# Kernel optimization log

Measured on AMD Instinct MI355X. Metric: run time of the kernel, lower is better.

Reference implementation:

```python
import jax, jax.numpy as jnp
import numpy as np

B, C = 8192, 128  # batch (edges/nodes), channels


def setup_inputs() -> dict:
    key = jax.random.key(0)
    k1, k2 = jax.random.split(key)
    T1 = jax.random.normal(k1, (B, C, 3, 3, 3), dtype=jnp.float32)
    T2 = jax.random.normal(k2, (B, C, 3, 3, 3), dtype=jnp.float32)
    return {"T1": T1, "T2": T2}


def reference(T1, T2):
    # BroadcastTC with r_1 = r_2 = 3 and three contractions (k = 1, 2, 3).
    # Original code permutes contracted axes of T1 to the back and of T2 to
    # the front, broadcasts an outer product, and sums the k contracted axes.
    # That is exactly a batched tensor contraction; we express it with einsum
    # (same math, no materialized broadcast product). Normalizer = 1/sqrt(3^k).
    # k=1: contract last axis of T1 with first feature axis of T2 -> rank-4 output
    out1 = jnp.einsum('bcxyk,bckuv->bcxyuv', T1, T2) * np.float32(1.0 / np.sqrt(3.0))
    # k=2: contract last two axes of T1 with first two feature axes of T2 -> rank-2
    out2 = jnp.einsum('bcxkl,bcklu->bcxu', T1, T2) * np.float32(1.0 / 3.0)
    # k=3: full contraction -> rank-0 (scalar per batch/channel)
    out3 = jnp.einsum('bcklm,bcklm->bc', T1, T2) * np.float32(1.0 / np.sqrt(27.0))
    return (out1, out2, out3)
```

## Files before the change

kernel.cpp:

```cpp
#include <hip/hip_runtime.h>


#define TPB 256
#define PPB 256

constexpr int  NPAIR    = 8192 * 128;
constexpr long OUT2_OFF = (long)NPAIR * 81;
constexpr long OUT3_OFF = OUT2_OFF + (long)NPAIR * 9;

__global__ __launch_bounds__(TPB)
void btc_kernel(const float* __restrict__ T1, const float* __restrict__ T2,
                float* __restrict__ out)
{
    __shared__ __align__(16) float lds[PPB * 27];

    const int  tid      = threadIdx.x;
    const long pairBase = (long)blockIdx.x * PPB;

    {
        const float4* g = reinterpret_cast<const float4*>(T1 + pairBase * 27);
        float4*       l = reinterpret_cast<float4*>(lds);
        #pragma unroll
        for (int i = 0; i < 7; ++i) {
            int idx = tid + i * TPB;
            if (idx < (PPB * 27) / 4) l[idx] = g[idx];
        }
    }
    __syncthreads();
    float a[27];
    #pragma unroll
    for (int j = 0; j < 27; ++j) a[j] = lds[tid * 27 + j];
    __syncthreads();

    {
        const float4* g = reinterpret_cast<const float4*>(T2 + pairBase * 27);
        float4*       l = reinterpret_cast<float4*>(lds);
        #pragma unroll
        for (int i = 0; i < 7; ++i) {
            int idx = tid + i * TPB;
            if (idx < (PPB * 27) / 4) l[idx] = g[idx];
        }
    }
    __syncthreads();
    float b[27];
    #pragma unroll
    for (int j = 0; j < 27; ++j) b[j] = lds[tid * 27 + j];
    __syncthreads();

    const float n1 = 0.57735026918962576f;
    const float n2 = 0.33333333333333333f;
    const float n3 = 0.19245008972987526f;

    #pragma unroll 1
    for (int g = 0; g < 4; ++g) {
        if ((tid >> 6) == g) {
            const int lp = tid & 63;
            #pragma unroll
            for (int x = 0; x < 3; ++x)
                #pragma unroll
                for (int y = 0; y < 3; ++y)
                    #pragma unroll
                    for (int u = 0; u < 3; ++u)
                        #pragma unroll
                        for (int v = 0; v < 3; ++v) {
                            float s = a[x*9 + y*3 + 0] * b[ 0 + u*3 + v]
                                    + a[x*9 + y*3 + 1] * b[ 9 + u*3 + v]
                                    + a[x*9 + y*3 + 2] * b[18 + u*3 + v];
                            lds[lp * 81 + x*27 + y*9 + u*3 + v] = s * n1;
                        }
        }
        __syncthreads();
        {
            const float4* ls = reinterpret_cast<const float4*>(lds);
            float4*       go = reinterpret_cast<float4*>(out + (pairBase + g * 64) * 81);
            #pragma unroll
            for (int k = 0; k < 6; ++k) {
                int idx = tid + k * TPB;
                if (idx < 1296) go[idx] = ls[idx];
            }
        }
        __syncthreads();
    }

    #pragma unroll
    for (int x = 0; x < 3; ++x) {
        #pragma unroll
        for (int u = 0; u < 3; ++u) {
            float s = 0.f;
            #pragma unroll
            for (int k = 0; k < 3; ++k)
                #pragma unroll
                for (int l = 0; l < 3; ++l)
                    s += a[x*9 + k*3 + l] * b[k*9 + l*3 + u];
            lds[tid * 9 + x*3 + u] = s * n2;
        }
    }
    __syncthreads();
    {
        const float4* ls = reinterpret_cast<const float4*>(lds);
        float4*       go = reinterpret_cast<float4*>(out + OUT2_OFF + pairBase * 9);
        #pragma unroll
        for (int k = 0; k < 3; ++k) {
            int idx = tid + k * TPB;
            if (idx < 576) go[idx] = ls[idx];
        }
    }

    float s3 = 0.f;
    #pragma unroll
    for (int j = 0; j < 27; ++j) s3 += a[j] * b[j];
    out[OUT3_OFF + pairBase + tid] = s3 * n3;
}

extern "C" void kernel_launch(void* const* d_in, const int* in_sizes, int n_in,
                              void* d_out, int out_size, void* d_ws, size_t ws_size,
                              hipStream_t stream)
{
    const float* T1  = (const float*)d_in[0];
    const float* T2  = (const float*)d_in[1];
    float*       out = (float*)d_out;

    dim3 grid(NPAIR / PPB);
    dim3 block(TPB);
    hipLaunchKernelGGL(btc_kernel, grid, block, 0, stream, T1, T2, out);
}
```

Baseline: 529.0 us.

## Use single-wavefront blocks with duplicated pair work to drop block barriers

Each block is now one 64-lane wavefront handling 32 pairs. Both lane halves redundantly compute each pair's contraction, and each half writes a different part of the rank-4 output into LDS. Because the block is a single wavefront, all __syncthreads barriers are removed, and the serialized four-group staging loop becomes one pass. The cost is doubled arithmetic and many more, smaller blocks. The design also relies on lockstep wavefront execution for LDS ordering without explicit barriers.

```diff
diff --git a/kernel.cpp b/kernel.cpp
--- a/kernel.cpp
+++ b/kernel.cpp
@@ -1,10 +1,10 @@
 #include <hip/hip_runtime.h>
 
 
-#define TPB 256
-#define PPB 256
+#define TPB 64
 
 constexpr int  NPAIR    = 8192 * 128;
+constexpr int  PPW      = 32;
 constexpr long OUT2_OFF = (long)NPAIR * 81;
 constexpr long OUT3_OFF = OUT2_OFF + (long)NPAIR * 9;
 
@@ -12,78 +12,61 @@
 void btc_kernel(const float* __restrict__ T1, const float* __restrict__ T2,
                 float* __restrict__ out)
 {
-    __shared__ __align__(16) float lds[PPB * 27];
+    __shared__ __align__(16) float buf[PPW * 81];
 
-    const int  tid      = threadIdx.x;
-    const long pairBase = (long)blockIdx.x * PPB;
+    const int  lane     = threadIdx.x;
+    const int  h        = lane >> 5;
+    const int  p        = lane & 31;
+    const long pairBase = (long)blockIdx.x * PPW;
 
     {
-        const float4* g = reinterpret_cast<const float4*>(T1 + pairBase * 27);
-        float4*       l = reinterpret_cast<float4*>(lds);
+        const float4* g1 = reinterpret_cast<const float4*>(T1 + pairBase * 27);
+        const float4* g2 = reinterpret_cast<const float4*>(T2 + pairBase * 27);
+        float4*       lb = reinterpret_cast<float4*>(buf);
         #pragma unroll
-        for (int i = 0; i < 7; ++i) {
-            int idx = tid + i * TPB;
-            if (idx < (PPB * 27) / 4) l[idx] = g[idx];
-        }
+        for (int r = 0; r < 3; ++r) lb[r * 64 + lane]       = g1[r * 64 + lane];
+        if (lane < 24)              lb[192 + lane]          = g1[192 + lane];
+        #pragma unroll
+        for (int r = 0; r < 3; ++r) lb[216 + r * 64 + lane] = g2[r * 64 + lane];
+        if (lane < 24)              lb[216 + 192 + lane]    = g2[192 + lane];
     }
-    __syncthreads();
-    float a[27];
+
+    float a[27], b[27];
     #pragma unroll
-    for (int j = 0; j < 27; ++j) a[j] = lds[tid * 27 + j];
-    __syncthreads();
-
-    {
-        const float4* g = reinterpret_cast<const float4*>(T2 + pairBase * 27);
-        float4*       l = reinterpret_cast<float4*>(lds);
-        #pragma unroll
-        for (int i = 0; i < 7; ++i) {
-            int idx = tid + i * TPB;
-            if (idx < (PPB * 27) / 4) l[idx] = g[idx];
-        }
-    }
-    __syncthreads();
-    float b[27];
+    for (int t = 0; t < 27; ++t) a[t] = buf[p * 27 + t];
     #pragma unroll
-    for (int j = 0; j < 27; ++j) b[j] = lds[tid * 27 + j];
-    __syncthreads();
+    for (int t = 0; t < 27; ++t) b[t] = buf[864 + p * 27 + t];
 
     const float n1 = 0.57735026918962576f;
     const float n2 = 0.33333333333333333f;
     const float n3 = 0.19245008972987526f;
 
-    #pragma unroll 1
-    for (int g = 0; g < 4; ++g) {
-        if ((tid >> 6) == g) {
-            const int lp = tid & 63;
+    #pragma unroll
+    for (int x = 0; x < 3; ++x)
+        #pragma unroll
+        for (int y = 0; y < 3; ++y)
             #pragma unroll
-            for (int x = 0; x < 3; ++x)
+            for (int u = 0; u < 3; ++u)
                 #pragma unroll
-                for (int y = 0; y < 3; ++y)
-                    #pragma unroll
-                    for (int u = 0; u < 3; ++u)
-                        #pragma unroll
-                        for (int v = 0; v < 3; ++v) {
-                            float s = a[x*9 + y*3 + 0] * b[ 0 + u*3 + v]
-                                    + a[x*9 + y*3 + 1] * b[ 9 + u*3 + v]
-                                    + a[x*9 + y*3 + 2] * b[18 + u*3 + v];
-                            lds[lp * 81 + x*27 + y*9 + u*3 + v] = s * n1;
-                        }
-        }
-        __syncthreads();
-        {
-            const float4* ls = reinterpret_cast<const float4*>(lds);
-            float4*       go = reinterpret_cast<float4*>(out + (pairBase + g * 64) * 81);
-            #pragma unroll
-            for (int k = 0; k < 6; ++k) {
-                int idx = tid + k * TPB;
-                if (idx < 1296) go[idx] = ls[idx];
-            }
-        }
-        __syncthreads();
+                for (int v = 0; v < 3; ++v) {
+                    const int j = x * 27 + y * 9 + u * 3 + v;
+                    float s = a[x*9 + y*3 + 0] * b[ 0 + u*3 + v]
+                            + a[x*9 + y*3 + 1] * b[ 9 + u*3 + v]
+                            + a[x*9 + y*3 + 2] * b[18 + u*3 + v];
+                    if ((j > 40) == (h == 1))
+                        buf[p * 81 + j] = s * n1;
+                }
+
+    {
+        const float4* lb = reinterpret_cast<const float4*>(buf);
+        float4*       go = reinterpret_cast<float4*>(out + pairBase * 81);
+        #pragma unroll
+        for (int r = 0; r < 10; ++r) go[r * 64 + lane] = lb[r * 64 + lane];
+        if (lane < 8)                go[640 + lane]    = lb[640 + lane];
     }
 
     #pragma unroll
-    for (int x = 0; x < 3; ++x) {
+    for (int x = 0; x < 3; ++x)
         #pragma unroll
         for (int u = 0; u < 3; ++u) {
             float s = 0.f;
@@ -92,24 +75,20 @@
                 #pragma unroll
                 for (int l = 0; l < 3; ++l)
                     s += a[x*9 + k*3 + l] * b[k*9 + l*3 + u];
-            lds[tid * 9 + x*3 + u] = s * n2;
+            if (h == 0) buf[p * 9 + x * 3 + u] = s * n2;
         }
-    }
-    __syncthreads();
+
     {
-        const float4* ls = reinterpret_cast<const float4*>(lds);
+        const float4* lb = reinterpret_cast<const float4*>(buf);
         float4*       go = reinterpret_cast<float4*>(out + OUT2_OFF + pairBase * 9);
-        #pragma unroll
-        for (int k = 0; k < 3; ++k) {
-            int idx = tid + k * TPB;
-            if (idx < 576) go[idx] = ls[idx];
-        }
+        go[lane] = lb[lane];
+        if (lane < 8) go[64 + lane] = lb[64 + lane];
     }
 
     float s3 = 0.f;
     #pragma unroll
-    for (int j = 0; j < 27; ++j) s3 += a[j] * b[j];
-    out[OUT3_OFF + pairBase + tid] = s3 * n3;
+    for (int t = 0; t < 27; ++t) s3 += a[t] * b[t];
+    if (h == 0) out[OUT3_OFF + pairBase + p] = s3 * n3;
 }
 
 extern "C" void kernel_launch(void* const* d_in, const int* in_sizes, int n_in,
@@ -120,7 +99,7 @@
     const float* T2  = (const float*)d_in[1];
     float*       out = (float*)d_out;
 
-    dim3 grid(NPAIR / PPB);
+    dim3 grid(NPAIR / PPW);
     dim3 block(TPB);
     hipLaunchKernelGGL(btc_kernel, grid, block, 0, stream, T1, T2, out);
 }
```

Result: faster. 511.3 us (-3.3%).
